# Performance work log

Hardware: AMD Instinct MI355X
Metric: run time of the kernel (lower is better)

The kernel has to match this reference:

```python
import jax, jax.numpy as jnp
import numpy as np

N = 20000      # nodes
E = 640000     # edges
IN = 2         # in_dim
H = 4          # heads
C = 64         # hidden_dim (per-head channels)
ED = 3         # edge_dim
K = 4          # num_clusters
EPS = 1e-16    # PyG softmax eps


def setup_inputs():
    key = jax.random.key(0)
    ks = jax.random.split(key, 32)
    g = lambda i, sh: (jax.random.normal(ks[i], sh, dtype=jnp.float32) * 0.1)
    inp = {
        'x': jax.random.normal(ks[0], (N, IN), dtype=jnp.float32),
        'edge_index': jax.random.randint(ks[1], (2, E), 0, N, dtype=jnp.int64),
        'edge_attr': jax.random.normal(ks[2], (E, ED), dtype=jnp.float32),
        # input_proj
        'Wp': g(3, (IN, C)), 'bp': g(4, (C,)),
        # conv1: in C -> H*C, concat
        'W1': g(5, (C, H * C)), 'We1': g(6, (ED, H * C)),
        'as1': g(7, (H, C)), 'ad1': g(8, (H, C)), 'ae1': g(9, (H, C)), 'b1': g(10, (H * C,)),
        # conv2: in H*C -> H*C, concat
        'W2': g(11, (H * C, H * C)), 'We2': g(12, (ED, H * C)),
        'as2': g(13, (H, C)), 'ad2': g(14, (H, C)), 'ae2': g(15, (H, C)), 'b2': g(16, (H * C,)),
        # conv3: in H*C -> C, heads=1
        'W3': g(17, (H * C, C)), 'We3': g(18, (ED, C)),
        'as3': g(19, (1, C)), 'ad3': g(20, (1, C)), 'ae3': g(21, (1, C)), 'b3': g(22, (C,)),
        # classifier
        'Wc': g(23, (C, K)), 'bc': g(24, (K,)),
    }
    return inp


def _gat(h, src, dst, edge_attr, W, We, a_src, a_dst, a_edge, bias, heads, cph):
    """PyG GATConv (shared lin for src/dst, edge_dim, concat=True), eval mode."""
    xh = (h @ W).reshape(N, heads, cph)                       # [N,H,C]
    alpha_src = jnp.einsum('nhc,hc->nh', xh, a_src)           # [N,H]
    alpha_dst = jnp.einsum('nhc,hc->nh', xh, a_dst)
    eh = (edge_attr @ We).reshape(E, heads, cph)              # [E,H,C]
    alpha = alpha_src[src] + alpha_dst[dst] + jnp.einsum('ehc,hc->eh', eh, a_edge)
    alpha = jax.nn.leaky_relu(alpha, 0.2)                     # [E,H]
    # segment softmax over destination neighborhoods
    m = jax.ops.segment_max(alpha, dst, num_segments=N)       # [N,H]
    ea = jnp.exp(alpha - m[dst])
    s = jax.ops.segment_sum(ea, dst, num_segments=N)
    attn = ea / (s[dst] + EPS)                                # [E,H]
    msg = xh[src] * attn[:, :, None]                          # [E,H,C]
    out = jax.ops.segment_sum(msg, dst, num_segments=N)       # [N,H,C]
    return out.reshape(N, heads * cph) + bias


def reference(x, edge_index, edge_attr, Wp, bp,
              W1, We1, as1, ad1, ae1, b1,
              W2, We2, as2, ad2, ae2, b2,
              W3, We3, as3, ad3, ae3, b3,
              Wc, bc):
    src, dst = edge_index[0], edge_index[1]
    h = jax.nn.elu(x @ Wp + bp)
    h = jax.nn.elu(_gat(h, src, dst, edge_attr, W1, We1, as1, ad1, ae1, b1, H, C))
    h = jax.nn.elu(_gat(h, src, dst, edge_attr, W2, We2, as2, ad2, ae2, b2, H, C))
    h = _gat(h, src, dst, edge_attr, W3, We3, as3, ad3, ae3, b3, 1, C)
    return jax.nn.softmax(h @ Wc + bc, axis=-1)
```

## Files before the change

kernel.cpp:

```cpp
#include <hip/hip_runtime.h>
#include <math.h>

#define N_NODES 20000
#define N_EDGES 640000

typedef __attribute__((ext_vector_type(8))) short short8;
typedef __attribute__((ext_vector_type(4))) float floatx4;

__device__ __forceinline__ float elu_f(float v) { return v > 0.f ? v : expm1f(v); }

__device__ __forceinline__ unsigned short bf16_rne(float f) {
  union { float f; unsigned u; } v;
  v.f = f;
  unsigned r = v.u + 0x7FFF + ((v.u >> 16) & 1);
  return (unsigned short)(r >> 16);
}

__device__ __forceinline__ float bf_to_f(unsigned short u) {
  union { unsigned u; float f; } v;
  v.u = (unsigned)u << 16;
  return v.f;
}


__global__ void zero_int_kernel(int* p, int n) {
  int i = blockIdx.x * 256 + threadIdx.x;
  if (i < n) p[i] = 0;
}

__global__ void hist_kernel(const int* __restrict__ dst, int* __restrict__ cnt, int ne) {
  int e = blockIdx.x * 256 + threadIdx.x;
  if (e < ne) atomicAdd(&cnt[dst[e]], 1);
}

__global__ __launch_bounds__(1024) void scan_kernel(const int* __restrict__ cnt,
                                                    int* __restrict__ row_ptr,
                                                    int* __restrict__ row_next, int n) {
  __shared__ int part[1024];
  int t = threadIdx.x;
  int per = (n + 1023) / 1024;
  int base = t * per;
  int local = 0;
  for (int i = 0; i < per; ++i) {
    int idx = base + i;
    if (idx < n) local += cnt[idx];
  }
  part[t] = local;
  __syncthreads();
  for (int off = 1; off < 1024; off <<= 1) {
    int v = (t >= off) ? part[t - off] : 0;
    __syncthreads();
    part[t] += v;
    __syncthreads();
  }
  int prefix = (t == 0) ? 0 : part[t - 1];
  for (int i = 0; i < per; ++i) {
    int idx = base + i;
    if (idx < n) {
      row_ptr[idx] = prefix;
      row_next[idx] = prefix;
      prefix += cnt[idx];
    }
  }
  if (t == 1023) row_ptr[n] = part[1023];
}

__global__ void fill_kernel(const int* __restrict__ src, const int* __restrict__ dst,
                            const float* __restrict__ ea, int* __restrict__ row_next,
                            int* __restrict__ csr_src, float* __restrict__ csr_ea, int ne) {
  int e = blockIdx.x * 256 + threadIdx.x;
  if (e >= ne) return;
  int d = dst[e];
  int pos = atomicAdd(&row_next[d], 1);
  csr_src[pos] = src[e];
  csr_ea[pos * 3 + 0] = ea[e * 3 + 0];
  csr_ea[pos * 3 + 1] = ea[e * 3 + 1];
  csr_ea[pos * 3 + 2] = ea[e * 3 + 2];
}


__global__ void wt_all_kernel(const float* __restrict__ W1, const float* __restrict__ W2,
                              const float* __restrict__ W3, unsigned short* __restrict__ Bt1,
                              unsigned short* __restrict__ Bt2, unsigned short* __restrict__ Bt3) {
  int idx = blockIdx.x * 256 + threadIdx.x;
  const float* W; unsigned short* Bt; int K, Nc, local;
  if (idx < 16384)      { W = W1; Bt = Bt1; K = 64;  Nc = 256; local = idx; }
  else if (idx < 81920) { W = W2; Bt = Bt2; K = 256; Nc = 256; local = idx - 16384; }
  else if (idx < 98304) { W = W3; Bt = Bt3; K = 256; Nc = 64;  local = idx - 81920; }
  else return;
  int k = local / Nc, n = local - k * Nc;
  Bt[(size_t)n * K + k] = bf16_rne(W[local]);
}


__global__ void aeproj_all_kernel(const float* __restrict__ We1, const float* __restrict__ ae1,
                                  const float* __restrict__ We2, const float* __restrict__ ae2,
                                  const float* __restrict__ We3, const float* __restrict__ ae3,
                                  float* __restrict__ proj) {
  int t = threadIdx.x;
  if (t < 12) {
    int d = t >> 2, h = t & 3;
    float s = 0.f;
    for (int c = 0; c < 64; ++c) s += We1[d * 256 + h * 64 + c] * ae1[h * 64 + c];
    proj[t] = s;
  } else if (t < 24) {
    int u = t - 12; int d = u >> 2, h = u & 3;
    float s = 0.f;
    for (int c = 0; c < 64; ++c) s += We2[d * 256 + h * 64 + c] * ae2[h * 64 + c];
    proj[t] = s;
  } else if (t < 27) {
    int d = t - 24;
    float s = 0.f;
    for (int c = 0; c < 64; ++c) s += We3[d * 64 + c] * ae3[c];
    proj[t] = s;
  }
}


__global__ void in_proj_kernel(const float* __restrict__ x, const float* __restrict__ Wp,
                               const float* __restrict__ bp, unsigned short* __restrict__ h_bf,
                               int n) {
  int i = blockIdx.x * 256 + threadIdx.x;
  if (i >= n * 64) return;
  int node = i >> 6, c = i & 63;
  float v = x[node * 2] * Wp[c] + x[node * 2 + 1] * Wp[64 + c] + bp[c];
  h_bf[i] = bf16_rne(elu_f(v));
}


template <int KDIM>
__global__ __launch_bounds__(256) void mfma_gemm_kernel(const unsigned short* __restrict__ A,
                                                        const unsigned short* __restrict__ Bt,
                                                        unsigned short* __restrict__ C_bf,
                                                        int M, int Nc) {
  __shared__ unsigned short As[64][40];
  __shared__ unsigned short Bs[64][40];
  int t = threadIdx.x;
  int wave = t >> 6, lane = t & 63;
  int m_frag = lane & 15, quad = lane >> 4;
  int row0 = blockIdx.y * 64, col0 = blockIdx.x * 64;
  int lr = t >> 2;
  int lk = (t & 3) * 8;
  floatx4 acc[4];
  #pragma unroll
  for (int c = 0; c < 4; ++c) acc[c] = (floatx4){0.f, 0.f, 0.f, 0.f};

  for (int k0 = 0; k0 < KDIM; k0 += 32) {
    int gr = row0 + lr;
    short8 av = {0, 0, 0, 0, 0, 0, 0, 0};
    if (gr < M) av = *(const short8*)(A + (size_t)gr * KDIM + k0 + lk);
    *(short8*)(&As[lr][lk]) = av;
    short8 bv = *(const short8*)(Bt + (size_t)(col0 + lr) * KDIM + k0 + lk);
    *(short8*)(&Bs[lr][lk]) = bv;
    __syncthreads();
    short8 a = *(const short8*)(&As[wave * 16 + m_frag][quad * 8]);
    #pragma unroll
    for (int c = 0; c < 4; ++c) {
      short8 b = *(const short8*)(&Bs[c * 16 + m_frag][quad * 8]);
      acc[c] = __builtin_amdgcn_mfma_f32_16x16x32_bf16(a, b, acc[c], 0, 0, 0);
    }
    __syncthreads();
  }
  #pragma unroll
  for (int c = 0; c < 4; ++c) {
    #pragma unroll
    for (int i = 0; i < 4; ++i) {
      int gr = row0 + wave * 16 + quad * 4 + i;
      if (gr < M) C_bf[(size_t)gr * Nc + col0 + c * 16 + m_frag] = bf16_rne(acc[c][i]);
    }
  }
}


__global__ void alpha_sd_kernel(const unsigned short* __restrict__ xh_bf,
                                const float* __restrict__ a_s, const float* __restrict__ a_d,
                                float* __restrict__ alpha_s, float* __restrict__ alpha_d,
                                int n_nodes, int heads) {
  int gid = blockIdx.x * 256 + threadIdx.x;
  int wid = gid >> 6, lane = gid & 63;
  if (wid >= n_nodes * heads) return;
  int h = wid % heads;
  float v = bf_to_f(xh_bf[(size_t)wid * 64 + lane]);
  float ps = v * a_s[h * 64 + lane];
  float pd = v * a_d[h * 64 + lane];
  for (int off = 32; off; off >>= 1) {
    ps += __shfl_down(ps, off);
    pd += __shfl_down(pd, off);
  }
  if (lane == 0) {
    alpha_s[wid] = ps;
    alpha_d[wid] = pd;
  }
}


template <int H>
__global__ __launch_bounds__(256) void fused_softmax_kernel(const int* __restrict__ row_ptr,
                                                            const int* __restrict__ csr_src,
                                                            const float* __restrict__ csr_ea,
                                                            const float* __restrict__ alp_s,
                                                            const float* __restrict__ alp_d,
                                                            const float* __restrict__ proj,
                                                            float* __restrict__ attn,
                                                            int n_nodes) {
  int t = threadIdx.x;
  int wave = t >> 6, lane = t & 63;
  int n, h;
  if (H == 4) { n = blockIdx.x; h = wave; }
  else        { n = blockIdx.x * 4 + wave; h = 0; if (n >= n_nodes) return; }
  int s0 = row_ptr[n], s1 = row_ptr[n + 1];
  float adv = alp_d[n * H + h];
  float p0 = proj[0 * H + h], p1 = proj[1 * H + h], p2 = proj[2 * H + h];
  float* __restrict__ plane = attn + (size_t)h * N_EDGES;
  float m = -INFINITY, ssum = 0.f;
  for (int i = s0 + lane; i < s1; i += 64) {
    int s = csr_src[i];
    float a = alp_s[s * H + h] + adv
            + csr_ea[i * 3 + 0] * p0 + csr_ea[i * 3 + 1] * p1 + csr_ea[i * 3 + 2] * p2;
    a = a > 0.f ? a : 0.2f * a;
    plane[i] = a;
    float nm = fmaxf(m, a);
    ssum = ssum * __expf(m - nm) + __expf(a - nm);
    m = nm;
  }
  #pragma unroll
  for (int off = 1; off < 64; off <<= 1) {
    float mo = __shfl_xor(m, off);
    float so = __shfl_xor(ssum, off);
    float nm = fmaxf(m, mo);
    if (nm > -INFINITY) {
      ssum = ssum * __expf(m - nm) + so * __expf(mo - nm);
      m = nm;
    }
  }
  float inv = 1.0f / (ssum + 1e-16f);
  for (int i = s0 + lane; i < s1; i += 64) {
    plane[i] = __expf(plane[i] - m) * inv;
  }
}


template <int HC, bool APPLY_ELU, bool OUT_BF>
__global__ __launch_bounds__(256) void aggregate_kernel(const int* __restrict__ row_ptr,
                                                        const int* __restrict__ csr_src,
                                                        const float* __restrict__ attn,
                                                        const unsigned short* __restrict__ xh_bf,
                                                        const float* __restrict__ bias,
                                                        float* __restrict__ out,
                                                        unsigned short* __restrict__ out_bf) {
  constexpr int L = HC / 8;
  constexpr int S = 256 / L;
  int n = blockIdx.x;
  int t = threadIdx.x;
  int slot = t / L;
  int l = t % L;
  int head = (8 * l) >> 6;
  int s0 = row_ptr[n], s1 = row_ptr[n + 1];
  const float* __restrict__ attn_h = attn + (size_t)head * N_EDGES;
  float acc[8] = {};
  for (int i = s0 + slot; i < s1; i += S) {
    int s = csr_src[i];
    float w = attn_h[i];
    short8 v = *(const short8*)(xh_bf + (size_t)s * HC + l * 8);
    #pragma unroll
    for (int j = 0; j < 8; ++j) acc[j] += bf_to_f((unsigned short)v[j]) * w;
  }
  __shared__ float red[S * HC];
  #pragma unroll
  for (int j = 0; j < 8; ++j) red[slot * HC + l * 8 + j] = acc[j];
  __syncthreads();
  if (t < HC) {
    float a = 0.f;
    #pragma unroll
    for (int s = 0; s < S; ++s) a += red[s * HC + t];
    a += bias[t];
    if (APPLY_ELU) a = elu_f(a);
    if (OUT_BF) out_bf[(size_t)n * HC + t] = bf16_rne(a);
    else        out[(size_t)n * HC + t] = a;
  }
}


__global__ void classifier_kernel(const float* __restrict__ h, const float* __restrict__ Wc,
                                  const float* __restrict__ bc, float* __restrict__ out,
                                  int n_nodes) {
  int gid = blockIdx.x * 256 + threadIdx.x;
  int w = gid >> 6, lane = gid & 63;
  if (w >= n_nodes) return;
  float hv = h[w * 64 + lane];
  float p0 = hv * Wc[lane * 4 + 0];
  float p1 = hv * Wc[lane * 4 + 1];
  float p2 = hv * Wc[lane * 4 + 2];
  float p3 = hv * Wc[lane * 4 + 3];
  for (int off = 32; off; off >>= 1) {
    p0 += __shfl_down(p0, off);
    p1 += __shfl_down(p1, off);
    p2 += __shfl_down(p2, off);
    p3 += __shfl_down(p3, off);
  }
  if (lane == 0) {
    p0 += bc[0]; p1 += bc[1]; p2 += bc[2]; p3 += bc[3];
    float mx = fmaxf(fmaxf(p0, p1), fmaxf(p2, p3));
    float e0 = __expf(p0 - mx), e1 = __expf(p1 - mx), e2 = __expf(p2 - mx), e3 = __expf(p3 - mx);
    float inv = 1.f / (e0 + e1 + e2 + e3);
    out[w * 4 + 0] = e0 * inv;
    out[w * 4 + 1] = e1 * inv;
    out[w * 4 + 2] = e2 * inv;
    out[w * 4 + 3] = e3 * inv;
  }
}


extern "C" void kernel_launch(void* const* d_in, const int* in_sizes, int n_in,
                              void* d_out, int out_size, void* d_ws, size_t ws_size,
                              hipStream_t stream) {
  const float* x   = (const float*)d_in[0];
  const int*   ei  = (const int*)d_in[1];
  const float* ea  = (const float*)d_in[2];
  const float* Wp  = (const float*)d_in[3];
  const float* bp  = (const float*)d_in[4];
  const float* W1  = (const float*)d_in[5];
  const float* We1 = (const float*)d_in[6];
  const float* as1 = (const float*)d_in[7];
  const float* ad1 = (const float*)d_in[8];
  const float* ae1 = (const float*)d_in[9];
  const float* b1  = (const float*)d_in[10];
  const float* W2  = (const float*)d_in[11];
  const float* We2 = (const float*)d_in[12];
  const float* as2 = (const float*)d_in[13];
  const float* ad2 = (const float*)d_in[14];
  const float* ae2 = (const float*)d_in[15];
  const float* b2  = (const float*)d_in[16];
  const float* W3  = (const float*)d_in[17];
  const float* We3 = (const float*)d_in[18];
  const float* as3 = (const float*)d_in[19];
  const float* ad3 = (const float*)d_in[20];
  const float* ae3 = (const float*)d_in[21];
  const float* b3  = (const float*)d_in[22];
  const float* Wc  = (const float*)d_in[23];
  const float* bc  = (const float*)d_in[24];
  float* out = (float*)d_out;

  const int* src = ei;
  const int* dst = ei + N_EDGES;

  char* wptr = (char*)d_ws;
  auto alloc = [&](size_t bytes) {
    char* p = wptr;
    wptr += (bytes + 255) & ~(size_t)255;
    return p;
  };
  int*            cnt      = (int*)alloc((size_t)N_NODES * 4);
  int*            row_ptr  = (int*)alloc((size_t)(N_NODES + 1) * 4);
  int*            row_next = (int*)alloc((size_t)N_NODES * 4);
  int*            csr_src  = (int*)alloc((size_t)N_EDGES * 4);
  float*          csr_ea   = (float*)alloc((size_t)N_EDGES * 3 * 4);
  unsigned short* hA_bf    = (unsigned short*)alloc((size_t)N_NODES * 256 * 2);
  unsigned short* hX_bf    = (unsigned short*)alloc((size_t)N_NODES * 256 * 2);
  float*          hC       = (float*)alloc((size_t)N_NODES * 64 * 4);
  float*          alp_s    = (float*)alloc((size_t)N_NODES * 4 * 4);
  float*          alp_d    = (float*)alloc((size_t)N_NODES * 4 * 4);
  float*          alp_e    = (float*)alloc((size_t)N_EDGES * 4 * 4);
  float*          proj     = (float*)alloc(32 * 4);
  unsigned short* Bt1      = (unsigned short*)alloc((size_t)64 * 256 * 2);
  unsigned short* Bt2      = (unsigned short*)alloc((size_t)256 * 256 * 2);
  unsigned short* Bt3      = (unsigned short*)alloc((size_t)256 * 64 * 2);

  zero_int_kernel<<<(N_NODES + 255) / 256, 256, 0, stream>>>(cnt, N_NODES);
  hist_kernel<<<(N_EDGES + 255) / 256, 256, 0, stream>>>(dst, cnt, N_EDGES);
  scan_kernel<<<1, 1024, 0, stream>>>(cnt, row_ptr, row_next, N_NODES);
  fill_kernel<<<(N_EDGES + 255) / 256, 256, 0, stream>>>(src, dst, ea, row_next,
                                                         csr_src, csr_ea, N_EDGES);

  wt_all_kernel<<<(98304 + 255) / 256, 256, 0, stream>>>(W1, W2, W3, Bt1, Bt2, Bt3);
  aeproj_all_kernel<<<1, 64, 0, stream>>>(We1, ae1, We2, ae2, We3, ae3, proj);

  in_proj_kernel<<<N_NODES * 64 / 256, 256, 0, stream>>>(x, Wp, bp, hA_bf, N_NODES);

  dim3 g256(4, (N_NODES + 63) / 64);
  dim3 g64(1, (N_NODES + 63) / 64);

  mfma_gemm_kernel<64><<<g256, 256, 0, stream>>>(hA_bf, Bt1, hX_bf, N_NODES, 256);
  alpha_sd_kernel<<<N_NODES * 4 * 64 / 256, 256, 0, stream>>>(hX_bf, as1, ad1, alp_s, alp_d, N_NODES, 4);
  fused_softmax_kernel<4><<<N_NODES, 256, 0, stream>>>(row_ptr, csr_src, csr_ea, alp_s, alp_d,
                                                       proj + 0, alp_e, N_NODES);
  aggregate_kernel<256, true, true><<<N_NODES, 256, 0, stream>>>(row_ptr, csr_src, alp_e, hX_bf,
                                                                 b1, nullptr, hA_bf);

  mfma_gemm_kernel<256><<<g256, 256, 0, stream>>>(hA_bf, Bt2, hX_bf, N_NODES, 256);
  alpha_sd_kernel<<<N_NODES * 4 * 64 / 256, 256, 0, stream>>>(hX_bf, as2, ad2, alp_s, alp_d, N_NODES, 4);
  fused_softmax_kernel<4><<<N_NODES, 256, 0, stream>>>(row_ptr, csr_src, csr_ea, alp_s, alp_d,
                                                       proj + 12, alp_e, N_NODES);
  aggregate_kernel<256, true, true><<<N_NODES, 256, 0, stream>>>(row_ptr, csr_src, alp_e, hX_bf,
                                                                 b2, nullptr, hA_bf);

  mfma_gemm_kernel<256><<<g64, 256, 0, stream>>>(hA_bf, Bt3, hX_bf, N_NODES, 64);
  alpha_sd_kernel<<<N_NODES * 1 * 64 / 256, 256, 0, stream>>>(hX_bf, as3, ad3, alp_s, alp_d, N_NODES, 1);
  fused_softmax_kernel<1><<<(N_NODES + 3) / 4, 256, 0, stream>>>(row_ptr, csr_src, csr_ea, alp_s,
                                                                 alp_d, proj + 24, alp_e, N_NODES);
  aggregate_kernel<64, false, false><<<N_NODES, 256, 0, stream>>>(row_ptr, csr_src, alp_e, hX_bf,
                                                                  b3, hC, nullptr);

  classifier_kernel<<<N_NODES * 64 / 256, 256, 0, stream>>>(hC, Wc, bc, out, N_NODES);
}
```

Measured before the change: 466.0 us.

## Fuse attention softmax into aggregation and alpha dot-products into GEMM epilogue

Attention logits, an online chunked softmax and the weighted neighbour aggregation now run in one kernel per layer, so the per-edge attention array is no longer written to and re-read from global memory. The alpha_src/alpha_dst dot products move into the MFMA GEMM epilogue, computed from fp32 accumulators, which drops a separate pass over xh. The CSR fill now stores only edge ids, so src and edge_attr are gathered indirectly in every layer. This adds extra scattered loads and block-wide syncs per chunk, and wave-level max/sum reductions for each chunk.

```diff
diff --git a/kernel.cpp b/kernel.cpp
--- a/kernel.cpp
+++ b/kernel.cpp
@@ -65,17 +65,12 @@
   if (t == 1023) row_ptr[n] = part[1023];
 }
 
-__global__ void fill_kernel(const int* __restrict__ src, const int* __restrict__ dst,
-                            const float* __restrict__ ea, int* __restrict__ row_next,
-                            int* __restrict__ csr_src, float* __restrict__ csr_ea, int ne) {
+__global__ void fill_kernel(const int* __restrict__ dst, int* __restrict__ row_next,
+                            int* __restrict__ csr_eid, int ne) {
   int e = blockIdx.x * 256 + threadIdx.x;
   if (e >= ne) return;
-  int d = dst[e];
-  int pos = atomicAdd(&row_next[d], 1);
-  csr_src[pos] = src[e];
-  csr_ea[pos * 3 + 0] = ea[e * 3 + 0];
-  csr_ea[pos * 3 + 1] = ea[e * 3 + 1];
-  csr_ea[pos * 3 + 2] = ea[e * 3 + 2];
+  int pos = atomicAdd(&row_next[dst[e]], 1);
+  csr_eid[pos] = e;
 }
 
 
@@ -129,10 +124,11 @@
 
 
 template <int KDIM>
-__global__ __launch_bounds__(256) void mfma_gemm_kernel(const unsigned short* __restrict__ A,
-                                                        const unsigned short* __restrict__ Bt,
-                                                        unsigned short* __restrict__ C_bf,
-                                                        int M, int Nc) {
+__global__ __launch_bounds__(256) void mfma_gemm_alpha_kernel(
+    const unsigned short* __restrict__ A, const unsigned short* __restrict__ Bt,
+    unsigned short* __restrict__ C_bf, const float* __restrict__ a_src,
+    const float* __restrict__ a_dst, float* __restrict__ alp_s,
+    float* __restrict__ alp_d, int M, int Nc) {
   __shared__ unsigned short As[64][40];
   __shared__ unsigned short Bs[64][40];
   int t = threadIdx.x;
@@ -161,6 +157,28 @@
     }
     __syncthreads();
   }
+
+  int H = Nc >> 6;
+  int head = blockIdx.x;
+  float ps[4] = {}, pd[4] = {};
+  #pragma unroll
+  for (int c = 0; c < 4; ++c) {
+    float asv = a_src[head * 64 + c * 16 + m_frag];
+    float adv = a_dst[head * 64 + c * 16 + m_frag];
+    #pragma unroll
+    for (int i = 0; i < 4; ++i) {
+      ps[i] += acc[c][i] * asv;
+      pd[i] += acc[c][i] * adv;
+    }
+  }
+  #pragma unroll
+  for (int off = 1; off < 16; off <<= 1) {
+    #pragma unroll
+    for (int i = 0; i < 4; ++i) {
+      ps[i] += __shfl_xor(ps[i], off);
+      pd[i] += __shfl_xor(pd[i], off);
+    }
+  }
   #pragma unroll
   for (int c = 0; c < 4; ++c) {
     #pragma unroll
@@ -169,105 +187,103 @@
       if (gr < M) C_bf[(size_t)gr * Nc + col0 + c * 16 + m_frag] = bf16_rne(acc[c][i]);
     }
   }
-}
-
-
-__global__ void alpha_sd_kernel(const unsigned short* __restrict__ xh_bf,
-                                const float* __restrict__ a_s, const float* __restrict__ a_d,
-                                float* __restrict__ alpha_s, float* __restrict__ alpha_d,
-                                int n_nodes, int heads) {
-  int gid = blockIdx.x * 256 + threadIdx.x;
-  int wid = gid >> 6, lane = gid & 63;
-  if (wid >= n_nodes * heads) return;
-  int h = wid % heads;
-  float v = bf_to_f(xh_bf[(size_t)wid * 64 + lane]);
-  float ps = v * a_s[h * 64 + lane];
-  float pd = v * a_d[h * 64 + lane];
-  for (int off = 32; off; off >>= 1) {
-    ps += __shfl_down(ps, off);
-    pd += __shfl_down(pd, off);
-  }
-  if (lane == 0) {
-    alpha_s[wid] = ps;
-    alpha_d[wid] = pd;
-  }
-}
-
-
-template <int H>
-__global__ __launch_bounds__(256) void fused_softmax_kernel(const int* __restrict__ row_ptr,
-                                                            const int* __restrict__ csr_src,
-                                                            const float* __restrict__ csr_ea,
-                                                            const float* __restrict__ alp_s,
-                                                            const float* __restrict__ alp_d,
-                                                            const float* __restrict__ proj,
-                                                            float* __restrict__ attn,
-                                                            int n_nodes) {
+  if (m_frag == 0) {
+    #pragma unroll
+    for (int i = 0; i < 4; ++i) {
+      int gr = row0 + wave * 16 + quad * 4 + i;
+      if (gr < M) {
+        alp_s[gr * H + head] = ps[i];
+        alp_d[gr * H + head] = pd[i];
+      }
+    }
+  }
+}
+
+
+template <int HC, bool APPLY_ELU, bool OUT_BF>
+__global__ __launch_bounds__(256) void softagg_kernel(
+    const int* __restrict__ row_ptr, const int* __restrict__ csr_eid,
+    const int* __restrict__ src_arr, const float* __restrict__ ea,
+    const float* __restrict__ alp_s, const float* __restrict__ alp_d,
+    const float* __restrict__ proj, const unsigned short* __restrict__ xh_bf,
+    const float* __restrict__ bias, float* __restrict__ out,
+    unsigned short* __restrict__ out_bf) {
+  constexpr int H = HC / 64;
+  constexpr int CHUNK = 256;
+  constexpr int L = HC / 8;
+  constexpr int S = 256 / L;
+  __shared__ float lds_w[H][CHUNK];
+  __shared__ int lds_src[CHUNK];
+  __shared__ float sh_r[H];
+  __shared__ float sh_inv[H];
+  __shared__ float red[S * HC];
+
+  int n = blockIdx.x;
   int t = threadIdx.x;
   int wave = t >> 6, lane = t & 63;
-  int n, h;
-  if (H == 4) { n = blockIdx.x; h = wave; }
-  else        { n = blockIdx.x * 4 + wave; h = 0; if (n >= n_nodes) return; }
+  int slot = t / L, l = t % L;
+  int head2 = (8 * l) >> 6;
   int s0 = row_ptr[n], s1 = row_ptr[n + 1];
-  float adv = alp_d[n * H + h];
-  float p0 = proj[0 * H + h], p1 = proj[1 * H + h], p2 = proj[2 * H + h];
-  float* __restrict__ plane = attn + (size_t)h * N_EDGES;
-  float m = -INFINITY, ssum = 0.f;
-  for (int i = s0 + lane; i < s1; i += 64) {
-    int s = csr_src[i];
-    float a = alp_s[s * H + h] + adv
-            + csr_ea[i * 3 + 0] * p0 + csr_ea[i * 3 + 1] * p1 + csr_ea[i * 3 + 2] * p2;
-    a = a > 0.f ? a : 0.2f * a;
-    plane[i] = a;
-    float nm = fmaxf(m, a);
-    ssum = ssum * __expf(m - nm) + __expf(a - nm);
-    m = nm;
-  }
+
+  float m_run = -INFINITY, s_run = 0.f;
+  float acc[8] = {};
+  float adv = 0.f, p0 = 0.f, p1 = 0.f, p2 = 0.f;
+  if (wave < H) {
+    adv = alp_d[n * H + wave];
+    p0 = proj[0 * H + wave];
+    p1 = proj[1 * H + wave];
+    p2 = proj[2 * H + wave];
+  }
+
+  for (int c0 = s0; c0 < s1; c0 += CHUNK) {
+    int cend = min(s1, c0 + CHUNK);
+    if (wave < H) {
+      int h = wave;
+      float cm = -INFINITY;
+      for (int i = c0 + lane; i < cend; i += 64) {
+        int eid = csr_eid[i];
+        int s = src_arr[eid];
+        if (h == 0) lds_src[i - c0] = s;
+        float a = alp_s[s * H + h] + adv
+                + ea[eid * 3 + 0] * p0 + ea[eid * 3 + 1] * p1 + ea[eid * 3 + 2] * p2;
+        a = a > 0.f ? a : 0.2f * a;
+        lds_w[h][i - c0] = a;
+        cm = fmaxf(cm, a);
+      }
+      #pragma unroll
+      for (int off = 1; off < 64; off <<= 1) cm = fmaxf(cm, __shfl_xor(cm, off));
+      float m_new = fmaxf(m_run, cm);
+      float r = __expf(m_run - m_new);
+      float se = 0.f;
+      for (int i = c0 + lane; i < cend; i += 64) {
+        float w = __expf(lds_w[h][i - c0] - m_new);
+        lds_w[h][i - c0] = w;
+        se += w;
+      }
+      #pragma unroll
+      for (int off = 1; off < 64; off <<= 1) se += __shfl_xor(se, off);
+      s_run = s_run * r + se;
+      m_run = m_new;
+      if (lane == 0) sh_r[h] = r;
+    }
+    __syncthreads();
+    float rr = sh_r[head2];
+    #pragma unroll
+    for (int j = 0; j < 8; ++j) acc[j] *= rr;
+    for (int i = c0 + slot; i < cend; i += S) {
+      float w = lds_w[head2][i - c0];
+      int s = lds_src[i - c0];
+      short8 v = *(const short8*)(xh_bf + (size_t)s * HC + l * 8);
+      #pragma unroll
+      for (int j = 0; j < 8; ++j) acc[j] += bf_to_f((unsigned short)v[j]) * w;
+    }
+    __syncthreads();
+  }
+  if (wave < H && lane == 0) sh_inv[wave] = 1.0f / (s_run + 1e-16f);
+  __syncthreads();
+  float inv = sh_inv[head2];
   #pragma unroll
-  for (int off = 1; off < 64; off <<= 1) {
-    float mo = __shfl_xor(m, off);
-    float so = __shfl_xor(ssum, off);
-    float nm = fmaxf(m, mo);
-    if (nm > -INFINITY) {
-      ssum = ssum * __expf(m - nm) + so * __expf(mo - nm);
-      m = nm;
-    }
-  }
-  float inv = 1.0f / (ssum + 1e-16f);
-  for (int i = s0 + lane; i < s1; i += 64) {
-    plane[i] = __expf(plane[i] - m) * inv;
-  }
-}
-
-
-template <int HC, bool APPLY_ELU, bool OUT_BF>
-__global__ __launch_bounds__(256) void aggregate_kernel(const int* __restrict__ row_ptr,
-                                                        const int* __restrict__ csr_src,
-                                                        const float* __restrict__ attn,
-                                                        const unsigned short* __restrict__ xh_bf,
-                                                        const float* __restrict__ bias,
-                                                        float* __restrict__ out,
-                                                        unsigned short* __restrict__ out_bf) {
-  constexpr int L = HC / 8;
-  constexpr int S = 256 / L;
-  int n = blockIdx.x;
-  int t = threadIdx.x;
-  int slot = t / L;
-  int l = t % L;
-  int head = (8 * l) >> 6;
-  int s0 = row_ptr[n], s1 = row_ptr[n + 1];
-  const float* __restrict__ attn_h = attn + (size_t)head * N_EDGES;
-  float acc[8] = {};
-  for (int i = s0 + slot; i < s1; i += S) {
-    int s = csr_src[i];
-    float w = attn_h[i];
-    short8 v = *(const short8*)(xh_bf + (size_t)s * HC + l * 8);
-    #pragma unroll
-    for (int j = 0; j < 8; ++j) acc[j] += bf_to_f((unsigned short)v[j]) * w;
-  }
-  __shared__ float red[S * HC];
-  #pragma unroll
-  for (int j = 0; j < 8; ++j) red[slot * HC + l * 8 + j] = acc[j];
+  for (int j = 0; j < 8; ++j) red[slot * HC + l * 8 + j] = acc[j] * inv;
   __syncthreads();
   if (t < HC) {
     float a = 0.f;
@@ -276,7 +292,7 @@
     a += bias[t];
     if (APPLY_ELU) a = elu_f(a);
     if (OUT_BF) out_bf[(size_t)n * HC + t] = bf16_rne(a);
-    else        out[(size_t)n * HC + t] = a;
+    else out[(size_t)n * HC + t] = a;
   }
 }
 
@@ -353,14 +369,12 @@
   int*            cnt      = (int*)alloc((size_t)N_NODES * 4);
   int*            row_ptr  = (int*)alloc((size_t)(N_NODES + 1) * 4);
   int*            row_next = (int*)alloc((size_t)N_NODES * 4);
-  int*            csr_src  = (int*)alloc((size_t)N_EDGES * 4);
-  float*          csr_ea   = (float*)alloc((size_t)N_EDGES * 3 * 4);
+  int*            csr_eid  = (int*)alloc((size_t)N_EDGES * 4);
   unsigned short* hA_bf    = (unsigned short*)alloc((size_t)N_NODES * 256 * 2);
   unsigned short* hX_bf    = (unsigned short*)alloc((size_t)N_NODES * 256 * 2);
   float*          hC       = (float*)alloc((size_t)N_NODES * 64 * 4);
   float*          alp_s    = (float*)alloc((size_t)N_NODES * 4 * 4);
   float*          alp_d    = (float*)alloc((size_t)N_NODES * 4 * 4);
-  float*          alp_e    = (float*)alloc((size_t)N_EDGES * 4 * 4);
   float*          proj     = (float*)alloc(32 * 4);
   unsigned short* Bt1      = (unsigned short*)alloc((size_t)64 * 256 * 2);
   unsigned short* Bt2      = (unsigned short*)alloc((size_t)256 * 256 * 2);
@@ -369,8 +383,7 @@
   zero_int_kernel<<<(N_NODES + 255) / 256, 256, 0, stream>>>(cnt, N_NODES);
   hist_kernel<<<(N_EDGES + 255) / 256, 256, 0, stream>>>(dst, cnt, N_EDGES);
   scan_kernel<<<1, 1024, 0, stream>>>(cnt, row_ptr, row_next, N_NODES);
-  fill_kernel<<<(N_EDGES + 255) / 256, 256, 0, stream>>>(src, dst, ea, row_next,
-                                                         csr_src, csr_ea, N_EDGES);
+  fill_kernel<<<(N_EDGES + 255) / 256, 256, 0, stream>>>(dst, row_next, csr_eid, N_EDGES);
 
   wt_all_kernel<<<(98304 + 255) / 256, 256, 0, stream>>>(W1, W2, W3, Bt1, Bt2, Bt3);
   aeproj_all_kernel<<<1, 64, 0, stream>>>(We1, ae1, We2, ae2, We3, ae3, proj);
@@ -380,26 +393,23 @@
   dim3 g256(4, (N_NODES + 63) / 64);
   dim3 g64(1, (N_NODES + 63) / 64);
 
-  mfma_gemm_kernel<64><<<g256, 256, 0, stream>>>(hA_bf, Bt1, hX_bf, N_NODES, 256);
-  alpha_sd_kernel<<<N_NODES * 4 * 64 / 256, 256, 0, stream>>>(hX_bf, as1, ad1, alp_s, alp_d, N_NODES, 4);
-  fused_softmax_kernel<4><<<N_NODES, 256, 0, stream>>>(row_ptr, csr_src, csr_ea, alp_s, alp_d,
-                                                       proj + 0, alp_e, N_NODES);
-  aggregate_kernel<256, true, true><<<N_NODES, 256, 0, stream>>>(row_ptr, csr_src, alp_e, hX_bf,
-                                                                 b1, nullptr, hA_bf);
-
-  mfma_gemm_kernel<256><<<g256, 256, 0, stream>>>(hA_bf, Bt2, hX_bf, N_NODES, 256);
-  alpha_sd_kernel<<<N_NODES * 4 * 64 / 256, 256, 0, stream>>>(hX_bf, as2, ad2, alp_s, alp_d, N_NODES, 4);
-  fused_softmax_kernel<4><<<N_NODES, 256, 0, stream>>>(row_ptr, csr_src, csr_ea, alp_s, alp_d,
-                                                       proj + 12, alp_e, N_NODES);
-  aggregate_kernel<256, true, true><<<N_NODES, 256, 0, stream>>>(row_ptr, csr_src, alp_e, hX_bf,
-                                                                 b2, nullptr, hA_bf);
-
-  mfma_gemm_kernel<256><<<g64, 256, 0, stream>>>(hA_bf, Bt3, hX_bf, N_NODES, 64);
-  alpha_sd_kernel<<<N_NODES * 1 * 64 / 256, 256, 0, stream>>>(hX_bf, as3, ad3, alp_s, alp_d, N_NODES, 1);
-  fused_softmax_kernel<1><<<(N_NODES + 3) / 4, 256, 0, stream>>>(row_ptr, csr_src, csr_ea, alp_s,
-                                                                 alp_d, proj + 24, alp_e, N_NODES);
-  aggregate_kernel<64, false, false><<<N_NODES, 256, 0, stream>>>(row_ptr, csr_src, alp_e, hX_bf,
-                                                                  b3, hC, nullptr);
+  mfma_gemm_alpha_kernel<64><<<g256, 256, 0, stream>>>(hA_bf, Bt1, hX_bf, as1, ad1,
+                                                       alp_s, alp_d, N_NODES, 256);
+  softagg_kernel<256, true, true><<<N_NODES, 256, 0, stream>>>(row_ptr, csr_eid, src, ea,
+                                                               alp_s, alp_d, proj + 0, hX_bf,
+                                                               b1, nullptr, hA_bf);
+
+  mfma_gemm_alpha_kernel<256><<<g256, 256, 0, stream>>>(hA_bf, Bt2, hX_bf, as2, ad2,
+                                                        alp_s, alp_d, N_NODES, 256);
+  softagg_kernel<256, true, true><<<N_NODES, 256, 0, stream>>>(row_ptr, csr_eid, src, ea,
+                                                               alp_s, alp_d, proj + 12, hX_bf,
+                                                               b2, nullptr, hA_bf);
+
+  mfma_gemm_alpha_kernel<256><<<g64, 256, 0, stream>>>(hA_bf, Bt3, hX_bf, as3, ad3,
+                                                       alp_s, alp_d, N_NODES, 64);
+  softagg_kernel<64, false, false><<<N_NODES, 256, 0, stream>>>(row_ptr, csr_eid, src, ea,
+                                                                alp_s, alp_d, proj + 24, hX_bf,
+                                                                b3, hC, nullptr);
 
   classifier_kernel<<<N_NODES * 64 / 256, 256, 0, stream>>>(hC, Wc, bc, out, N_NODES);
 }
```

After: 423.2 us. 1.1x faster.
